# Kernel optimization log

Hardware: AMD Instinct MI355X
Metric: run time of the kernel (lower is better)

Reference implementation:

```python
import jax, jax.numpy as jnp
import numpy as np

INPUT_DIM = 24
HIDDEN = 128
NUM_LAYERS = 3
OUTPUT_DIM = 1


def _lstm_layer(x, Wih, Whh, bih, bhh):
    """Single LSTM layer, PyTorch gate order (i, f, g, o). x: [B,T,D] -> [B,T,H]."""
    B = x.shape[0]
    H = Whh.shape[1]
    # Precompute input projections for all timesteps at once: [B,T,4H]
    xg = jnp.einsum('btd,gd->btg', x, Wih) + bih
    xg = jnp.swapaxes(xg, 0, 1)  # [T,B,4H]
    h0 = jnp.zeros((B, H), x.dtype)
    c0 = jnp.zeros((B, H), x.dtype)

    def step(carry, xt):
        h, c = carry
        gates = xt + h @ Whh.T + bhh  # [B,4H]
        i, f, g, o = jnp.split(gates, 4, axis=-1)
        i = jax.nn.sigmoid(i)
        f = jax.nn.sigmoid(f)
        g = jnp.tanh(g)
        o = jax.nn.sigmoid(o)
        c = f * c + i * g
        h = o * jnp.tanh(c)
        return (h, c), h

    _, hs = jax.lax.scan(step, (h0, c0), xg)  # hs: [T,B,H]
    return jnp.swapaxes(hs, 0, 1)  # [B,T,H]


def setup_inputs() -> dict:
    key = jax.random.key(0)
    ks = jax.random.split(key, 16)
    B, T = 2048, 256
    s = 0.05
    inp = {
        'x': jax.random.normal(ks[0], (B, T, INPUT_DIM), dtype=jnp.float32),
    }
    dims_in = [INPUT_DIM, HIDDEN, HIDDEN]
    for l in range(NUM_LAYERS):
        inp[f'Wih{l}'] = jax.random.normal(ks[1 + 4 * l], (4 * HIDDEN, dims_in[l]), dtype=jnp.float32) * s
        inp[f'Whh{l}'] = jax.random.normal(ks[2 + 4 * l], (4 * HIDDEN, HIDDEN), dtype=jnp.float32) * s
        inp[f'bih{l}'] = jax.random.normal(ks[3 + 4 * l], (4 * HIDDEN,), dtype=jnp.float32) * s
        inp[f'bhh{l}'] = jax.random.normal(ks[4 + 4 * l], (4 * HIDDEN,), dtype=jnp.float32) * s
    inp['Wfc'] = jax.random.normal(ks[13], (OUTPUT_DIM, HIDDEN), dtype=jnp.float32) * s
    inp['bfc'] = jax.random.normal(ks[14], (OUTPUT_DIM,), dtype=jnp.float32) * s
    return inp


def reference(x, Wih0, Whh0, bih0, bhh0, Wih1, Whh1, bih1, bhh1,
              Wih2, Whh2, bih2, bhh2, Wfc, bfc):
    # 3 stacked LSTM layers (dropout inactive in eval mode), zero initial state.
    h = _lstm_layer(x, Wih0, Whh0, bih0, bhh0)
    h = _lstm_layer(h, Wih1, Whh1, bih1, bhh1)
    h = _lstm_layer(h, Wih2, Whh2, bih2, bhh2)
    # Linear projection of the final timestep: [B,1]
    return h[:, -1, :] @ Wfc.T + bfc
```

## Files before the change

### kernel.cpp

```cpp
#include <hip/hip_runtime.h>

#define T_STEPS 256
#define BATCH   2048
#define HID     128
#define ROWS    8
#define BH      (BATCH * HID)

typedef short short8  __attribute__((ext_vector_type(8)));
typedef float float4v __attribute__((ext_vector_type(4)));

__device__ __forceinline__ unsigned short f2bf(float f) {
    unsigned int u = __builtin_bit_cast(unsigned int, f);
    u += 0x7fffu + ((u >> 16) & 1u);
    return (unsigned short)(u >> 16);
}
__device__ __forceinline__ float bf2f(unsigned short b) {
    unsigned int u = ((unsigned int)b) << 16;
    return __builtin_bit_cast(float, u);
}

#if __has_builtin(__builtin_amdgcn_exp2f)
#define EXP2F(x) __builtin_amdgcn_exp2f(x)
#else
#define EXP2F(x) exp2f(x)
#endif
__device__ __forceinline__ float sigf(float x) {
    return __builtin_amdgcn_rcpf(1.0f + EXP2F(x * -1.442695041f));
}
__device__ __forceinline__ float tanh_fast(float x) {
    return 2.0f * __builtin_amdgcn_rcpf(1.0f + EXP2F(x * -2.885390082f)) - 1.0f;
}

__device__ __forceinline__ void block_sync_lds() {
    asm volatile("s_waitcnt lgkmcnt(0)" ::: "memory");
    __builtin_amdgcn_s_barrier();
    __builtin_amdgcn_sched_barrier(0);
}

__device__ __forceinline__ int lposH(int row, int off) {
    return row * 256 + (off ^ ((row & 7) << 4));
}
__device__ __forceinline__ int lposX(int row, int off) {
    return row * 256 + (off ^ ((row & 7) << 4));
}
__device__ __forceinline__ int lposX0(int row, int off) {
    return row * 64 + (off ^ ((row & 3) << 4));
}

__device__ __forceinline__ short8 load_w8(const float* __restrict__ p) {
    float4v a = *reinterpret_cast<const float4v*>(p);
    float4v b = *reinterpret_cast<const float4v*>(p + 4);
    short8 r;
    r[0] = (short)f2bf(a[0]); r[1] = (short)f2bf(a[1]);
    r[2] = (short)f2bf(a[2]); r[3] = (short)f2bf(a[3]);
    r[4] = (short)f2bf(b[0]); r[5] = (short)f2bf(b[1]);
    r[6] = (short)f2bf(b[2]); r[7] = (short)f2bf(b[3]);
    return r;
}

#define LDS_BYTES 12288

template<bool IS_L0, bool WRITE_H, bool FINAL>
__device__ __forceinline__ void lstm_phase(
    unsigned char* a_lds,
    const float* __restrict__ x0,
    const float* __restrict__ Wih,
    const float* __restrict__ Whh,
    const float* __restrict__ bih,
    const float* __restrict__ bhh,
    unsigned short* __restrict__ hbuf,
    const float* __restrict__ Wfc,
    const float* __restrict__ bfc,
    float* __restrict__ out,
    const int tid, const int b0)
{
    constexpr int XKS = IS_L0 ? 1 : 4;
    constexpr int XRB = IS_L0 ? 64 : 256;
    constexpr int HB  = ROWS * 256;
    constexpr int XB  = 16 * XRB;
    const int XS0 = 2 * HB, XS1 = 2 * HB + XB;

    const int lane = tid & 63;
    const int wv   = tid >> 6;

    const int t16   = lane & 15;
    const int kgrp8 = (lane >> 4) * 8;
    const int jcol  = 16 * wv + t16;
    const int row0  = ((lane >> 4) & 1) * 4 + ((lane >> 5) & 1) * 2;

    const int g2   = t16 >> 2;
    const int hrow = ((g2 & 1) << 2) | ((g2 >> 1) << 1) | (t16 & 1);
    int aoffH[4];
    #pragma unroll
    for (int ks = 0; ks < 4; ++ks)
        aoffH[ks] = lposH(hrow, ks * 64 + kgrp8 * 2);
    int aoffX[XKS];
    #pragma unroll
    for (int s = 0; s < XKS; ++s)
        aoffX[s] = IS_L0 ? lposX0(t16, kgrp8 * 2)
                         : lposX(t16, s * 64 + kgrp8 * 2);

    const int hwoff0 = lposH(row0,     2 * jcol);
    const int hwoff1 = lposH(row0 + 1, 2 * jcol);

    const int sh_row = (tid >> 5) & 7, sh_c8 = tid & 31;
    const int hroff8 = lposH(sh_row, sh_c8 * 8);
    const size_t sgoff8 = (size_t)(b0 + sh_row) * HID + sh_c8 * 4;

    const int tid2 = tid & 255;
    const int sar = tid2 >> 4, sc16 = tid2 & 15;
    const int sb  = (sar & 1) | (((sar >> 3) & 1) << 1) | (((sar >> 2) & 1) << 2);
    const int ss  = (sar >> 1) & 1;
    const int xwoff = lposX(sar, sc16 * 16);
    const size_t xgrow = (size_t)(b0 + sb) * HID + sc16 * 8;
    const bool xvalid = (sc16 < 12);
    const int xw0off = lposX0(sar, sc16 * 4);
    const size_t x0row = (size_t)(b0 + sb) * (T_STEPS * 24) + sc16 * 2;

    short8 wfh[4][4], wfx[4][XKS];
    float  bias[4];
    #pragma unroll
    for (int q = 0; q < 4; ++q) {
        const int n = 128 * q + jcol;
        bias[q] = bih[n] + bhh[n];
        #pragma unroll
        for (int ks = 0; ks < 4; ++ks)
            wfh[q][ks] = load_w8(Whh + n * 128 + ks * 32 + kgrp8);
        if (IS_L0) {
            if (kgrp8 < 24) wfx[q][0] = load_w8(Wih + n * 24 + kgrp8);
            else            { short8 z = {0,0,0,0,0,0,0,0}; wfx[q][0] = z; }
        } else {
            #pragma unroll
            for (int s = 0; s < 4; ++s)
                wfx[q][s] = load_w8(Wih + n * 128 + s * 32 + kgrp8);
        }
    }

    {
        short8 z = {0,0,0,0,0,0,0,0};
        #pragma unroll
        for (int i = 0; i < 2; ++i) {
            const int a = tid * 16 + i * 8192;
            if (a < LDS_BYTES)
                *reinterpret_cast<short8*>(&a_lds[a]) = z;
        }
    }
    __syncthreads();

    short8 xpre = {0,0,0,0,0,0,0,0};
    float2 xpf  = {0.f, 0.f};
    if (tid >= 256) {
        if (!IS_L0) {
            short8 v0 = *reinterpret_cast<const short8*>(&hbuf[(size_t)(0 + ss) * BH + xgrow]);
            short8 v1 = *reinterpret_cast<const short8*>(&hbuf[(size_t)(2 + ss) * BH + xgrow]);
            *reinterpret_cast<short8*>(&a_lds[XS0 + xwoff]) = v0;
            *reinterpret_cast<short8*>(&a_lds[XS1 + xwoff]) = v1;
            xpre = *reinterpret_cast<const short8*>(&hbuf[(size_t)(4 + ss) * BH + xgrow]);
        } else if (xvalid) {
            float2 a = *reinterpret_cast<const float2*>(&x0[x0row + (size_t)(0 + ss) * 24]);
            float2 b = *reinterpret_cast<const float2*>(&x0[x0row + (size_t)(2 + ss) * 24]);
            unsigned int pa, pb;
            asm("v_cvt_pk_bf16_f32 %0, %1, %2" : "=v"(pa) : "v"(a.x), "v"(a.y));
            asm("v_cvt_pk_bf16_f32 %0, %1, %2" : "=v"(pb) : "v"(b.x), "v"(b.y));
            *reinterpret_cast<unsigned int*>(&a_lds[XS0 + xw0off]) = pa;
            *reinterpret_cast<unsigned int*>(&a_lds[XS1 + xw0off]) = pb;
            xpf = *reinterpret_cast<const float2*>(&x0[x0row + (size_t)(4 + ss) * 24]);
        }
    }
    __syncthreads();

    float4v xgA[4], xgB[4];
    #pragma unroll
    for (int q = 0; q < 4; ++q) {
        xgA[q] = float4v{bias[q], bias[q], bias[q], bias[q]};
        xgB[q] = float4v{bias[q], bias[q], bias[q], bias[q]};
    }
    {
        short8 xa[XKS];
        #pragma unroll
        for (int s = 0; s < XKS; ++s)
            xa[s] = *reinterpret_cast<const short8*>(&a_lds[XS0 + aoffX[s]]);
        #pragma unroll
        for (int s = 0; s < XKS; ++s)
            #pragma unroll
            for (int q = 0; q < 4; ++q)
                xgA[q] = __builtin_amdgcn_mfma_f32_16x16x32_bf16(xa[s], wfx[q][s], xgA[q], 0, 0, 0);
    }
    block_sync_lds();

    float creg[2] = {0.f, 0.f};

    auto cell_write = [&](float4v (&acc)[4], int wb) {
        const float c0 = sigf(acc[1][0]) * creg[0] + sigf(acc[0][0]) * tanh_fast(acc[2][0]);
        const float c1 = sigf(acc[1][1]) * creg[1] + sigf(acc[0][1]) * tanh_fast(acc[2][1]);
        creg[0] = c0;  creg[1] = c1;
        const float h0 = sigf(acc[3][0]) * tanh_fast(c0);
        const float h1 = sigf(acc[3][1]) * tanh_fast(c1);
        unsigned int packed;
        asm("v_cvt_pk_bf16_f32 %0, %1, %2" : "=v"(packed) : "v"(h0), "v"(h1));
        *reinterpret_cast<unsigned short*>(&a_lds[wb + hwoff0]) =
            (unsigned short)(packed & 0xffffu);
        *reinterpret_cast<unsigned short*>(&a_lds[wb + hwoff1]) =
            (unsigned short)(packed >> 16);
    };

    auto stepE = [&](int t, float4v (&cons)[4], float4v (&bld)[4],
                     const int XRD, const int XST) {
        short8 hva[4];
        #pragma unroll
        for (int ks = 0; ks < 4; ++ks)
            hva[ks] = *reinterpret_cast<const short8*>(&a_lds[0 + aoffH[ks]]);
        short8 xa0, xa1;
        if constexpr (!IS_L0) {
            xa0 = *reinterpret_cast<const short8*>(&a_lds[XRD + aoffX[0]]);
            xa1 = *reinterpret_cast<const short8*>(&a_lds[XRD + aoffX[1]]);
        } else {
            xa0 = *reinterpret_cast<const short8*>(&a_lds[XRD + aoffX[0]]);
        }
        float4v acc[4];
        #pragma unroll
        for (int q = 0; q < 4; ++q) {
            const float a = cons[q][0], b = cons[q][1];
            acc[q] = float4v{a, b, a, b};
        }
        if (tid < 256) {
            if (WRITE_H && t > 0) {
                int2 hv = *reinterpret_cast<const int2*>(&a_lds[0 + hroff8]);
                *reinterpret_cast<int2*>(&hbuf[(size_t)(t - 1) * BH + sgoff8]) = hv;
            }
        } else {
            if constexpr (!IS_L0) {
                *reinterpret_cast<short8*>(&a_lds[XST + xwoff]) = xpre;
            } else {
                if (xvalid) {
                    unsigned int p;
                    asm("v_cvt_pk_bf16_f32 %0, %1, %2" : "=v"(p) : "v"(xpf.x), "v"(xpf.y));
                    *reinterpret_cast<unsigned int*>(&a_lds[XST + xw0off]) = p;
                }
            }
        }
        __builtin_amdgcn_s_setprio(1);
        #pragma unroll
        for (int ks = 0; ks < 4; ++ks)
            #pragma unroll
            for (int q = 0; q < 4; ++q)
                acc[q] = __builtin_amdgcn_mfma_f32_16x16x32_bf16(hva[ks], wfh[q][ks], acc[q], 0, 0, 0);
        #pragma unroll
        for (int q = 0; q < 4; ++q)
            bld[q] = float4v{bias[q], bias[q], bias[q], bias[q]};
        if constexpr (!IS_L0) {
            #pragma unroll
            for (int q = 0; q < 4; ++q)
                bld[q] = __builtin_amdgcn_mfma_f32_16x16x32_bf16(xa0, wfx[q][0], bld[q], 0, 0, 0);
            #pragma unroll
            for (int q = 0; q < 4; ++q)
                bld[q] = __builtin_amdgcn_mfma_f32_16x16x32_bf16(xa1, wfx[q][1], bld[q], 0, 0, 0);
        } else {
            #pragma unroll
            for (int q = 0; q < 4; ++q)
                bld[q] = __builtin_amdgcn_mfma_f32_16x16x32_bf16(xa0, wfx[q][0], bld[q], 0, 0, 0);
        }
        __builtin_amdgcn_s_setprio(0);
        cell_write(acc, HB);
        block_sync_lds();
    };

    auto stepO = [&](int t, float4v (&cons)[4], float4v (&bld)[4],
                     const int XRD) {
        short8 hva[4];
        #pragma unroll
        for (int ks = 0; ks < 4; ++ks)
            hva[ks] = *reinterpret_cast<const short8*>(&a_lds[HB + aoffH[ks]]);
        short8 xa2, xa3;
        if constexpr (!IS_L0) {
            xa2 = *reinterpret_cast<const short8*>(&a_lds[XRD + aoffX[2]]);
            xa3 = *reinterpret_cast<const short8*>(&a_lds[XRD + aoffX[3]]);
        }
        float4v acc[4];
        #pragma unroll
        for (int q = 0; q < 4; ++q) {
            const float a = cons[q][2], b = cons[q][3];
            acc[q] = float4v{a, b, a, b};
        }
        if (tid < 256) {
            if (WRITE_H) {
                int2 hv = *reinterpret_cast<const int2*>(&a_lds[HB + hroff8]);
                *reinterpret_cast<int2*>(&hbuf[(size_t)(t - 1) * BH + sgoff8]) = hv;
            }
        } else {
            int tl = t + 5 + ss;
            tl = (tl < T_STEPS) ? tl : (T_STEPS - 1);
            if constexpr (!IS_L0) {
                xpre = *reinterpret_cast<const short8*>(&hbuf[(size_t)tl * BH + xgrow]);
            } else {
                if (xvalid)
                    xpf = *reinterpret_cast<const float2*>(&x0[x0row + (size_t)tl * 24]);
            }
        }
        __builtin_amdgcn_s_setprio(1);
        #pragma unroll
        for (int ks = 0; ks < 4; ++ks)
            #pragma unroll
            for (int q = 0; q < 4; ++q)
                acc[q] = __builtin_amdgcn_mfma_f32_16x16x32_bf16(hva[ks], wfh[q][ks], acc[q], 0, 0, 0);
        if constexpr (!IS_L0) {
            #pragma unroll
            for (int q = 0; q < 4; ++q)
                bld[q] = __builtin_amdgcn_mfma_f32_16x16x32_bf16(xa2, wfx[q][2], bld[q], 0, 0, 0);
            #pragma unroll
            for (int q = 0; q < 4; ++q)
                bld[q] = __builtin_amdgcn_mfma_f32_16x16x32_bf16(xa3, wfx[q][3], bld[q], 0, 0, 0);
        }
        __builtin_amdgcn_s_setprio(0);
        cell_write(acc, 0);
        block_sync_lds();
    };

    for (int q4 = 0; q4 < T_STEPS / 4; ++q4) {
        const int t0 = 4 * q4;
        stepE(t0,     xgA, xgB, XS1, XS0);
        stepO(t0 + 1, xgA, xgB, XS1);
        stepE(t0 + 2, xgB, xgA, XS0, XS1);
        stepO(t0 + 3, xgB, xgA, XS0);
    }
    if (WRITE_H && tid < 256) {
        int2 hv = *reinterpret_cast<const int2*>(&a_lds[0 + hroff8]);
        *reinterpret_cast<int2*>(&hbuf[(size_t)(T_STEPS - 1) * BH + sgoff8]) = hv;
    }
    if (FINAL && tid < 128) {
        const int r = tid >> 4, seg = tid & 15;
        float s = 0.f;
        #pragma unroll
        for (int k = 0; k < 8; ++k) {
            const int j = seg * 8 + k;
            s += bf2f(*reinterpret_cast<const unsigned short*>(&a_lds[lposH(r, 2 * j)]))
                 * Wfc[j];
        }
        #pragma unroll
        for (int off = 8; off >= 1; off >>= 1) s += __shfl_xor(s, off);
        if (seg == 0) out[b0 + r] = s + bfc[0];
    }
}

__global__ __launch_bounds__(512, 2)
void lstm3(const float* __restrict__ x0,
           const float* __restrict__ Wih0, const float* __restrict__ Whh0,
           const float* __restrict__ bih0, const float* __restrict__ bhh0,
           const float* __restrict__ Wih1, const float* __restrict__ Whh1,
           const float* __restrict__ bih1, const float* __restrict__ bhh1,
           const float* __restrict__ Wih2, const float* __restrict__ Whh2,
           const float* __restrict__ bih2, const float* __restrict__ bhh2,
           const float* __restrict__ Wfc,  const float* __restrict__ bfc,
           unsigned short* __restrict__ hbuf, float* __restrict__ out)
{
    __shared__ __attribute__((aligned(16))) unsigned char a_lds[LDS_BYTES];
    const int tid = threadIdx.x;
    const int b0  = blockIdx.x * ROWS;

    lstm_phase<true,  true,  false>(a_lds, x0, Wih0, Whh0, bih0, bhh0, hbuf,
                                    nullptr, nullptr, nullptr, tid, b0);
    __syncthreads();
    lstm_phase<false, true,  false>(a_lds, nullptr, Wih1, Whh1, bih1, bhh1, hbuf,
                                    nullptr, nullptr, nullptr, tid, b0);
    __syncthreads();
    lstm_phase<false, false, true >(a_lds, nullptr, Wih2, Whh2, bih2, bhh2, hbuf,
                                    Wfc, bfc, out, tid, b0);
}

extern "C" void kernel_launch(void* const* d_in, const int* in_sizes, int n_in,
                              void* d_out, int out_size, void* d_ws, size_t ws_size,
                              hipStream_t stream) {
    (void)in_sizes; (void)n_in; (void)out_size; (void)ws_size;
    const float* x    = (const float*)d_in[0];
    const float* Wih0 = (const float*)d_in[1];
    const float* Whh0 = (const float*)d_in[2];
    const float* bih0 = (const float*)d_in[3];
    const float* bhh0 = (const float*)d_in[4];
    const float* Wih1 = (const float*)d_in[5];
    const float* Whh1 = (const float*)d_in[6];
    const float* bih1 = (const float*)d_in[7];
    const float* bhh1 = (const float*)d_in[8];
    const float* Wih2 = (const float*)d_in[9];
    const float* Whh2 = (const float*)d_in[10];
    const float* bih2 = (const float*)d_in[11];
    const float* bhh2 = (const float*)d_in[12];
    const float* Wfc  = (const float*)d_in[13];
    const float* bfc  = (const float*)d_in[14];
    float* out = (float*)d_out;
    unsigned short* hbuf = (unsigned short*)d_ws;

    dim3 grid(BATCH / ROWS), block(512);
    lstm3<<<grid, block, 0, stream>>>(x, Wih0, Whh0, bih0, bhh0,
                                      Wih1, Whh1, bih1, bhh1,
                                      Wih2, Whh2, bih2, bhh2,
                                      Wfc, bfc, hbuf, out);
}
```

Measured before the change: 599.9 us.

## Move cell nonlinearity ahead of x-projection MFMAs and reschedule prefetch

Merges the even and odd step lambdas into one templated step. The gate activation and h write now run right after the recurrent MFMAs, and the next-step input projection MFMAs are issued afterwards, so that work can overlap the transcendental math and the barrier. The global prefetch moves from odd to even steps with a shorter lookahead, and the x-operand LDS reads move later. The barrier after the initial projection is also dropped, which risks an LDS race if that barrier guarded the first h reads.

```diff
diff --git a/kernel.cpp b/kernel.cpp
--- a/kernel.cpp
+++ b/kernel.cpp
@@ -8,6 +8,8 @@
 
 typedef short short8  __attribute__((ext_vector_type(8)));
 typedef float float4v __attribute__((ext_vector_type(4)));
+
+template<int P> struct IntC { static constexpr int value = P; };
 
 __device__ __forceinline__ unsigned short f2bf(float f) {
     unsigned int u = __builtin_bit_cast(unsigned int, f);
@@ -186,56 +188,54 @@
             for (int q = 0; q < 4; ++q)
                 xgA[q] = __builtin_amdgcn_mfma_f32_16x16x32_bf16(xa[s], wfx[q][s], xgA[q], 0, 0, 0);
     }
-    block_sync_lds();
 
     float creg[2] = {0.f, 0.f};
 
-    auto cell_write = [&](float4v (&acc)[4], int wb) {
-        const float c0 = sigf(acc[1][0]) * creg[0] + sigf(acc[0][0]) * tanh_fast(acc[2][0]);
-        const float c1 = sigf(acc[1][1]) * creg[1] + sigf(acc[0][1]) * tanh_fast(acc[2][1]);
-        creg[0] = c0;  creg[1] = c1;
-        const float h0 = sigf(acc[3][0]) * tanh_fast(c0);
-        const float h1 = sigf(acc[3][1]) * tanh_fast(c1);
-        unsigned int packed;
-        asm("v_cvt_pk_bf16_f32 %0, %1, %2" : "=v"(packed) : "v"(h0), "v"(h1));
-        *reinterpret_cast<unsigned short*>(&a_lds[wb + hwoff0]) =
-            (unsigned short)(packed & 0xffffu);
-        *reinterpret_cast<unsigned short*>(&a_lds[wb + hwoff1]) =
-            (unsigned short)(packed >> 16);
-    };
-
-    auto stepE = [&](int t, float4v (&cons)[4], float4v (&bld)[4],
-                     const int XRD, const int XST) {
+    auto do_step = [&](int t, auto PC) {
+        constexpr int POS = decltype(PC)::value;
+        constexpr bool EVEN = (POS & 1) == 0;
+        const int rb = EVEN ? 0 : HB;
+        const int wb = EVEN ? HB : 0;
+        float4v (&cons)[4] = (POS < 2) ? xgA : xgB;
+        float4v (&bld)[4]  = (POS < 2) ? xgB : xgA;
+        const int XRD = (POS < 2) ? XS1 : XS0;
+        const int XWR = (POS == 1) ? XS0 : XS1;
+
         short8 hva[4];
         #pragma unroll
         for (int ks = 0; ks < 4; ++ks)
-            hva[ks] = *reinterpret_cast<const short8*>(&a_lds[0 + aoffH[ks]]);
-        short8 xa0, xa1;
-        if constexpr (!IS_L0) {
-            xa0 = *reinterpret_cast<const short8*>(&a_lds[XRD + aoffX[0]]);
-            xa1 = *reinterpret_cast<const short8*>(&a_lds[XRD + aoffX[1]]);
-        } else {
-            xa0 = *reinterpret_cast<const short8*>(&a_lds[XRD + aoffX[0]]);
-        }
+            hva[ks] = *reinterpret_cast<const short8*>(&a_lds[rb + aoffH[ks]]);
         float4v acc[4];
         #pragma unroll
         for (int q = 0; q < 4; ++q) {
-            const float a = cons[q][0], b = cons[q][1];
+            const float a = EVEN ? cons[q][0] : cons[q][2];
+            const float b = EVEN ? cons[q][1] : cons[q][3];
             acc[q] = float4v{a, b, a, b};
         }
         if (tid < 256) {
             if (WRITE_H && t > 0) {
-                int2 hv = *reinterpret_cast<const int2*>(&a_lds[0 + hroff8]);
+                int2 hv = *reinterpret_cast<const int2*>(&a_lds[rb + hroff8]);
                 *reinterpret_cast<int2*>(&hbuf[(size_t)(t - 1) * BH + sgoff8]) = hv;
             }
         } else {
-            if constexpr (!IS_L0) {
-                *reinterpret_cast<short8*>(&a_lds[XST + xwoff]) = xpre;
+            if constexpr (EVEN) {
+                int tl = t + 4 + ss;
+                tl = (tl < T_STEPS) ? tl : (T_STEPS - 1);
+                if constexpr (!IS_L0) {
+                    xpre = *reinterpret_cast<const short8*>(&hbuf[(size_t)tl * BH + xgrow]);
+                } else {
+                    if (xvalid)
+                        xpf = *reinterpret_cast<const float2*>(&x0[x0row + (size_t)tl * 24]);
+                }
             } else {
-                if (xvalid) {
-                    unsigned int p;
-                    asm("v_cvt_pk_bf16_f32 %0, %1, %2" : "=v"(p) : "v"(xpf.x), "v"(xpf.y));
-                    *reinterpret_cast<unsigned int*>(&a_lds[XST + xw0off]) = p;
+                if constexpr (!IS_L0) {
+                    *reinterpret_cast<short8*>(&a_lds[XWR + xwoff]) = xpre;
+                } else {
+                    if (xvalid) {
+                        unsigned int p;
+                        asm("v_cvt_pk_bf16_f32 %0, %1, %2" : "=v"(p) : "v"(xpf.x), "v"(xpf.y));
+                        *reinterpret_cast<unsigned int*>(&a_lds[XWR + xw0off]) = p;
+                    }
                 }
             }
         }
@@ -245,83 +245,63 @@
             #pragma unroll
             for (int q = 0; q < 4; ++q)
                 acc[q] = __builtin_amdgcn_mfma_f32_16x16x32_bf16(hva[ks], wfh[q][ks], acc[q], 0, 0, 0);
-        #pragma unroll
-        for (int q = 0; q < 4; ++q)
-            bld[q] = float4v{bias[q], bias[q], bias[q], bias[q]};
+        __builtin_amdgcn_s_setprio(0);
+        {
+            const float c0 = sigf(acc[1][0]) * creg[0] + sigf(acc[0][0]) * tanh_fast(acc[2][0]);
+            const float c1 = sigf(acc[1][1]) * creg[1] + sigf(acc[0][1]) * tanh_fast(acc[2][1]);
+            creg[0] = c0;  creg[1] = c1;
+            const float h0 = sigf(acc[3][0]) * tanh_fast(c0);
+            const float h1 = sigf(acc[3][1]) * tanh_fast(c1);
+            unsigned int packed;
+            asm("v_cvt_pk_bf16_f32 %0, %1, %2" : "=v"(packed) : "v"(h0), "v"(h1));
+            *reinterpret_cast<unsigned short*>(&a_lds[wb + hwoff0]) =
+                (unsigned short)(packed & 0xffffu);
+            *reinterpret_cast<unsigned short*>(&a_lds[wb + hwoff1]) =
+                (unsigned short)(packed >> 16);
+        }
         if constexpr (!IS_L0) {
-            #pragma unroll
-            for (int q = 0; q < 4; ++q)
-                bld[q] = __builtin_amdgcn_mfma_f32_16x16x32_bf16(xa0, wfx[q][0], bld[q], 0, 0, 0);
-            #pragma unroll
-            for (int q = 0; q < 4; ++q)
-                bld[q] = __builtin_amdgcn_mfma_f32_16x16x32_bf16(xa1, wfx[q][1], bld[q], 0, 0, 0);
+            if constexpr (EVEN) {
+                short8 xa0 = *reinterpret_cast<const short8*>(&a_lds[XRD + aoffX[0]]);
+                short8 xa1 = *reinterpret_cast<const short8*>(&a_lds[XRD + aoffX[1]]);
+                #pragma unroll
+                for (int q = 0; q < 4; ++q)
+                    bld[q] = float4v{bias[q], bias[q], bias[q], bias[q]};
+                #pragma unroll
+                for (int q = 0; q < 4; ++q)
+                    bld[q] = __builtin_amdgcn_mfma_f32_16x16x32_bf16(xa0, wfx[q][0], bld[q], 0, 0, 0);
+                #pragma unroll
+                for (int q = 0; q < 4; ++q)
+                    bld[q] = __builtin_amdgcn_mfma_f32_16x16x32_bf16(xa1, wfx[q][1], bld[q], 0, 0, 0);
+            } else {
+                short8 xa2 = *reinterpret_cast<const short8*>(&a_lds[XRD + aoffX[2]]);
+                short8 xa3 = *reinterpret_cast<const short8*>(&a_lds[XRD + aoffX[3]]);
+                #pragma unroll
+                for (int q = 0; q < 4; ++q)
+                    bld[q] = __builtin_amdgcn_mfma_f32_16x16x32_bf16(xa2, wfx[q][2], bld[q], 0, 0, 0);
+                #pragma unroll
+                for (int q = 0; q < 4; ++q)
+                    bld[q] = __builtin_amdgcn_mfma_f32_16x16x32_bf16(xa3, wfx[q][3], bld[q], 0, 0, 0);
+            }
         } else {
-            #pragma unroll
-            for (int q = 0; q < 4; ++q)
-                bld[q] = __builtin_amdgcn_mfma_f32_16x16x32_bf16(xa0, wfx[q][0], bld[q], 0, 0, 0);
-        }
-        __builtin_amdgcn_s_setprio(0);
-        cell_write(acc, HB);
+            if constexpr (EVEN) {
+                short8 xa0 = *reinterpret_cast<const short8*>(&a_lds[XRD + aoffX[0]]);
+                #pragma unroll
+                for (int q = 0; q < 4; ++q)
+                    bld[q] = float4v{bias[q], bias[q], bias[q], bias[q]};
+                #pragma unroll
+                for (int q = 0; q < 4; ++q)
+                    bld[q] = __builtin_amdgcn_mfma_f32_16x16x32_bf16(xa0, wfx[q][0], bld[q], 0, 0, 0);
+            }
+        }
         block_sync_lds();
     };
 
-    auto stepO = [&](int t, float4v (&cons)[4], float4v (&bld)[4],
-                     const int XRD) {
-        short8 hva[4];
-        #pragma unroll
-        for (int ks = 0; ks < 4; ++ks)
-            hva[ks] = *reinterpret_cast<const short8*>(&a_lds[HB + aoffH[ks]]);
-        short8 xa2, xa3;
-        if constexpr (!IS_L0) {
-            xa2 = *reinterpret_cast<const short8*>(&a_lds[XRD + aoffX[2]]);
-            xa3 = *reinterpret_cast<const short8*>(&a_lds[XRD + aoffX[3]]);
-        }
-        float4v acc[4];
-        #pragma unroll
-        for (int q = 0; q < 4; ++q) {
-            const float a = cons[q][2], b = cons[q][3];
-            acc[q] = float4v{a, b, a, b};
-        }
-        if (tid < 256) {
-            if (WRITE_H) {
-                int2 hv = *reinterpret_cast<const int2*>(&a_lds[HB + hroff8]);
-                *reinterpret_cast<int2*>(&hbuf[(size_t)(t - 1) * BH + sgoff8]) = hv;
-            }
-        } else {
-            int tl = t + 5 + ss;
-            tl = (tl < T_STEPS) ? tl : (T_STEPS - 1);
-            if constexpr (!IS_L0) {
-                xpre = *reinterpret_cast<const short8*>(&hbuf[(size_t)tl * BH + xgrow]);
-            } else {
-                if (xvalid)
-                    xpf = *reinterpret_cast<const float2*>(&x0[x0row + (size_t)tl * 24]);
-            }
-        }
-        __builtin_amdgcn_s_setprio(1);
-        #pragma unroll
-        for (int ks = 0; ks < 4; ++ks)
-            #pragma unroll
-            for (int q = 0; q < 4; ++q)
-                acc[q] = __builtin_amdgcn_mfma_f32_16x16x32_bf16(hva[ks], wfh[q][ks], acc[q], 0, 0, 0);
-        if constexpr (!IS_L0) {
-            #pragma unroll
-            for (int q = 0; q < 4; ++q)
-                bld[q] = __builtin_amdgcn_mfma_f32_16x16x32_bf16(xa2, wfx[q][2], bld[q], 0, 0, 0);
-            #pragma unroll
-            for (int q = 0; q < 4; ++q)
-                bld[q] = __builtin_amdgcn_mfma_f32_16x16x32_bf16(xa3, wfx[q][3], bld[q], 0, 0, 0);
-        }
-        __builtin_amdgcn_s_setprio(0);
-        cell_write(acc, 0);
-        block_sync_lds();
-    };
-
-    for (int q4 = 0; q4 < T_STEPS / 4; ++q4) {
-        const int t0 = 4 * q4;
-        stepE(t0,     xgA, xgB, XS1, XS0);
-        stepO(t0 + 1, xgA, xgB, XS1);
-        stepE(t0 + 2, xgB, xgA, XS0, XS1);
-        stepO(t0 + 3, xgB, xgA, XS0);
+    for (int m = 0; m < T_STEPS / 4; ++m) {
+        const int t0 = 4 * m;
+        do_step(t0,     IntC<0>{});
+        do_step(t0 + 1, IntC<1>{});
+        do_step(t0 + 2, IntC<2>{});
+        do_step(t0 + 3, IntC<3>{});
     }
     if (WRITE_H && tid < 256) {
         int2 hv = *reinterpret_cast<const int2*>(&a_lds[0 + hroff8]);
```

Measured after the change: 573.4 us. 4.4% less time.
